# Performance work log

Measured on AMD Instinct MI355X. Metric: run time of the kernel, lower is better.

Reference implementation:

```python
import jax, jax.numpy as jnp
import numpy as np

N_NODES = 100000


def setup_inputs() -> dict:
    key = jax.random.key(0)
    k1, k2, k3, k4, k5 = jax.random.split(key, 5)
    n_feat, n_class = 128, 64
    E = 3200000
    x = jax.random.normal(k1, (N_NODES, n_feat), dtype=jnp.float32)
    edge_index = jax.random.randint(k2, (2, E), 0, N_NODES, dtype=jnp.int64)
    edge_weight = jax.random.uniform(k3, (E,), dtype=jnp.float32)
    # GCNConv params: glorot weight [in, out], zero-init bias (use small random for a non-trivial check)
    limit = float(np.sqrt(6.0 / (n_feat + n_class)))
    W = jax.random.uniform(k4, (n_feat, n_class), dtype=jnp.float32, minval=-limit, maxval=limit)
    b = jax.random.normal(k5, (n_class,), dtype=jnp.float32) * 0.01
    return {"x": x, "edge_index": edge_index, "edge_weight": edge_weight, "W": W, "b": b}


def _gcn_norm(edge_index, edge_weight, n):
    # add self-loops with weight 1 (PyG default fill_value=1.0)
    loop = jnp.arange(n, dtype=edge_index.dtype)
    row = jnp.concatenate([edge_index[0], loop])
    col = jnp.concatenate([edge_index[1], loop])
    w = jnp.concatenate([edge_weight, jnp.ones((n,), dtype=edge_weight.dtype)])
    deg = jax.ops.segment_sum(w, col, num_segments=n)  # in-degree by weight
    dis = jnp.where(deg > 0, jax.lax.rsqrt(jnp.where(deg > 0, deg, 1.0)), 0.0)
    norm = dis[row] * w * dis[col]
    return row, col, norm


def reference(x, edge_index, edge_weight, W, b):
    n = x.shape[0]
    row, col, norm = _gcn_norm(edge_index, edge_weight, n)
    h = x @ W  # linear transform before propagation, as in PyG GCNConv
    # gather source messages, scale by norm, scatter-add into targets
    msgs = h[row] * norm[:, None]          # [E+N, n_class]
    out = jax.ops.segment_sum(msgs, col, num_segments=n)
    return jax.nn.sigmoid(out + b)
```

## Files before the change

### kernel.cpp

```cpp
#include <hip/hip_runtime.h>
#include <hip/hip_bf16.h>
#include <math.h>


#define BLK 256
#define BBLK 1024
#define ABLK 1024
#define NBINBLK 512
#define NGRP 8
#define NB  512
#define CAPG 1024
#define CPB_MAX 200
#define PAD 76

typedef unsigned long long u64;
typedef unsigned int u32;
typedef unsigned short u16;
typedef unsigned char u8;
typedef _Float16 half8 __attribute__((ext_vector_type(8)));
typedef float f32x4 __attribute__((ext_vector_type(4)));

__global__ __launch_bounds__(BLK) void k_prep(const float* __restrict__ W,
                                              u16* __restrict__ WT,
                                              u32* __restrict__ cursor) {
    int gid = blockIdx.x * BLK + threadIdx.x;
    int gsz = gridDim.x * BLK;
    for (int i = gid; i < NB * NGRP; i += gsz) cursor[i] = 0u;
    for (int i = gid; i < 64 * 128; i += gsz) {
        int nn = i >> 7, k = i & 127;
        _Float16 h = (_Float16)W[k * 64 + nn];
        WT[nn * 128 + k] = *(u16*)&h;
    }
}

__global__ __launch_bounds__(BBLK) void k_bin(const int* __restrict__ row,
                                              const int* __restrict__ col,
                                              const float* __restrict__ w,
                                              u32* cursor,
                                              u64* __restrict__ staged,
                                              int E, int cpb, int nbins, int bpb) {
    __shared__ u32 hist[NB];
    __shared__ u32 sbase[NB];
    int t = threadIdx.x;
    int grp = blockIdx.x & (NGRP - 1);
    for (int j = t; j < NB; j += BBLK) hist[j] = 0;
    __syncthreads();
    int e0 = blockIdx.x * bpb;
    int e1 = min(e0 + bpb, E);
    int e = e0 + t;
    for (; e + 3 * BBLK < e1; e += 4 * BBLK) {
        int c0 = col[e];
        int c1 = col[e + BBLK];
        int c2 = col[e + 2 * BBLK];
        int c3 = col[e + 3 * BBLK];
        atomicAdd(&hist[(u32)c0 / (u32)cpb], 1u);
        atomicAdd(&hist[(u32)c1 / (u32)cpb], 1u);
        atomicAdd(&hist[(u32)c2 / (u32)cpb], 1u);
        atomicAdd(&hist[(u32)c3 / (u32)cpb], 1u);
    }
    for (; e < e1; e += BBLK)
        atomicAdd(&hist[(u32)col[e] / (u32)cpb], 1u);
    __syncthreads();
    for (int j = t; j < nbins; j += BBLK) {
        u32 h = hist[j];
        sbase[j] = h ? atomicAdd(&cursor[j * NGRP + grp], h) : 0u;
        hist[j] = 0u;
    }
    __syncthreads();
    e = e0 + t;
    for (; e + 3 * BBLK < e1; e += 4 * BBLK) {
#pragma unroll
        for (int j = 0; j < 4; j++) {
            int ee = e + j * BBLK;
            u32 c = (u32)col[ee];
            u32 bin = c / (u32)cpb;
            u32 colrel = c - bin * (u32)cpb;
            u32 wfix = (u32)(w[ee] * 65535.0f + 0.5f);
            u32 rel = sbase[bin] + atomicAdd(&hist[bin], 1u);
            if (rel < (u32)CAPG)
                staged[((size_t)bin * NGRP + grp) * CAPG + rel] =
                    (u64)((u32)row[ee] & 0xFFFFFu) | ((u64)colrel << 20)
                    | ((u64)wfix << 32);
        }
    }
    for (; e < e1; e += BBLK) {
        u32 c = (u32)col[e];
        u32 bin = c / (u32)cpb;
        u32 colrel = c - bin * (u32)cpb;
        u32 wfix = (u32)(w[e] * 65535.0f + 0.5f);
        u32 rel = sbase[bin] + atomicAdd(&hist[bin], 1u);
        if (rel < (u32)CAPG)
            staged[((size_t)bin * NGRP + grp) * CAPG + rel] =
                (u64)((u32)row[e] & 0xFFFFFu) | ((u64)colrel << 20)
                | ((u64)wfix << 32);
    }
}

__global__ __launch_bounds__(BLK) void k_deg(const u32* __restrict__ cursor,
                                             const u64* __restrict__ staged,
                                             float* __restrict__ dis,
                                             int N, int cpb) {
    __shared__ u32 deg[CPB_MAX];
    int bin = blockIdx.x, t = threadIdx.x;
    if (t < CPB_MAX) deg[t] = 0u;
    __syncthreads();
    for (int g = 0; g < NGRP; g++) {
        int ne = min((int)cursor[bin * NGRP + g], CAPG);
        size_t base = ((size_t)bin * NGRP + g) * CAPG;
        for (int i = t; i < ne; i += BLK) {
            u64 s = staged[base + i];
            atomicAdd(&deg[(u32)(s >> 20) & 0xFFFu], (u32)(s >> 32));
        }
    }
    __syncthreads();
    for (int j = t; j < cpb; j += BLK) {
        int c = bin * cpb + j;
        if (c < N)
            dis[c] = rsqrtf(1.0f + (float)deg[j] * (1.0f / 65535.0f));
    }
}

static __device__ __forceinline__ u16 f2bf(float f) {
    __hip_bfloat16 h = __float2bfloat16(f);
    return *(u16*)&h;
}

__global__ __launch_bounds__(BLK) void k_gemmM(const float* __restrict__ x,
                                               const u16* __restrict__ WT,
                                               const float* __restrict__ dis,
                                               u16* __restrict__ hs, int n) {
    __shared__ __attribute__((aligned(16))) _Float16 sx[64 * 136];
    __shared__ __attribute__((aligned(16))) _Float16 sw[64 * 136];
    __shared__ float sdis[64];
    int t = threadIdx.x;
    int m0 = blockIdx.x * 64;
    for (int i = t; i < 2048; i += BLK) {
        int r = i >> 5, q = i & 31;
        int gr = m0 + r;
        float4 v = make_float4(0.f, 0.f, 0.f, 0.f);
        if (gr < n) v = ((const float4*)x)[(size_t)gr * 32 + q];
        _Float16* dst = &sx[r * 136 + q * 4];
        dst[0] = (_Float16)v.x; dst[1] = (_Float16)v.y;
        dst[2] = (_Float16)v.z; dst[3] = (_Float16)v.w;
    }
    for (int i = t; i < 2048; i += BLK) {
        int nn = i >> 5, q = i & 31;
        ushort4 v = ((const ushort4*)WT)[nn * 32 + q];
        u16* dst = (u16*)&sw[nn * 136 + q * 4];
        dst[0] = v.x; dst[1] = v.y; dst[2] = v.z; dst[3] = v.w;
    }
    if (t < 64) sdis[t] = (m0 + t < n) ? dis[m0 + t] : 0.f;
    __syncthreads();
    int wv = t >> 6, lane = t & 63;
    int quad = lane >> 4, l16 = lane & 15;
    int mrow = wv * 16 + l16;
    half8 af[4];
#pragma unroll
    for (int kt = 0; kt < 4; kt++)
        af[kt] = *(const half8*)&sx[mrow * 136 + kt * 32 + quad * 8];
#pragma unroll
    for (int n0t = 0; n0t < 4; n0t++) {
        f32x4 acc = {0.f, 0.f, 0.f, 0.f};
#pragma unroll
        for (int kt = 0; kt < 4; kt++) {
            half8 bf_ = *(const half8*)&sw[(n0t * 16 + l16) * 136 + kt * 32 + quad * 8];
            acc = __builtin_amdgcn_mfma_f32_16x16x32_f16(af[kt], bf_, acc, 0, 0, 0);
        }
#pragma unroll
        for (int r = 0; r < 4; r++) {
            int mr = wv * 16 + quad * 4 + r;
            int gr = m0 + mr;
            if (gr < n)
                hs[(size_t)gr * 64 + n0t * 16 + l16] = f2bf(acc[r] * sdis[mr]);
        }
    }
}

__global__ __launch_bounds__(ABLK) void k_buildagg(const u32* __restrict__ cursor,
                                                   const u64* __restrict__ staged,
                                                   const uint2* __restrict__ hs64,
                                                   const float* __restrict__ dis,
                                                   const float* __restrict__ b,
                                                   float* __restrict__ out,
                                                   int N, int cpb) {
    __shared__ u32 cnt[CPB_MAX];
    __shared__ u32 lbkt[CPB_MAX * PAD];
    int bin = blockIdx.x, t = threadIdx.x;
    if (t < CPB_MAX) cnt[t] = 0u;
    __syncthreads();
    for (int g = 0; g < NGRP; g++) {
        int ne = min((int)cursor[bin * NGRP + g], CAPG);
        size_t base = ((size_t)bin * NGRP + g) * CAPG;
        for (int i = t; i < ne; i += ABLK) {
            u64 s = staged[base + i];
            u32 colrel = (u32)(s >> 20) & 0xFFFu;
            u32 wfix = (u32)(s >> 32);
            u32 rk = atomicAdd(&cnt[colrel], 1u);
            if (rk < (u32)PAD)
                lbkt[colrel * PAD + rk] = ((u32)s & 0xFFFFFu) | ((wfix >> 1) << 17);
        }
    }
    __syncthreads();
    int wv = t >> 6;
    int lane = t & 63;
    int q = lane >> 4, fp = lane & 15;
    const float WS = 1.0f / 32767.0f;
    for (int colrel = wv; colrel < cpb; colrel += (ABLK / 64)) {
        int node = bin * cpb + colrel;
        if (node >= N) break;
        int cc = (int)cnt[colrel];
        if (cc > PAD) cc = PAD;
        const u32* bkt = &lbkt[colrel * PAD];
        float a0, a1, a2, a3;
        if (q == 0) {
            uint2 s = hs64[((size_t)node << 4) + fp];
            a0 = __uint_as_float(s.x << 16);
            a1 = __uint_as_float(s.x & 0xFFFF0000u);
            a2 = __uint_as_float(s.y << 16);
            a3 = __uint_as_float(s.y & 0xFFFF0000u);
        } else {
            a0 = a1 = a2 = a3 = 0.f;
        }
        for (int e = 0; e < cc; e += 4) {
            int idx = e + q;
            u32 p = (idx < cc) ? bkt[idx] : 0u;
            float w = (float)(p >> 17) * WS;
            uint2 g = hs64[((size_t)(p & 0x1FFFFu) << 4) + fp];
            a0 = fmaf(__uint_as_float(g.x << 16), w, a0);
            a1 = fmaf(__uint_as_float(g.x & 0xFFFF0000u), w, a1);
            a2 = fmaf(__uint_as_float(g.y << 16), w, a2);
            a3 = fmaf(__uint_as_float(g.y & 0xFFFF0000u), w, a3);
        }
        a0 += __shfl_down(a0, 16); a1 += __shfl_down(a1, 16);
        a2 += __shfl_down(a2, 16); a3 += __shfl_down(a3, 16);
        a0 += __shfl_down(a0, 32); a1 += __shfl_down(a1, 32);
        a2 += __shfl_down(a2, 32); a3 += __shfl_down(a3, 32);
        if (q == 0) {
            float d = dis[node];
            float4 bv = ((const float4*)b)[fp];
            float4 o;
            o.x = 1.0f / (1.0f + __expf(-(d * a0 + bv.x)));
            o.y = 1.0f / (1.0f + __expf(-(d * a1 + bv.y)));
            o.z = 1.0f / (1.0f + __expf(-(d * a2 + bv.z)));
            o.w = 1.0f / (1.0f + __expf(-(d * a3 + bv.w)));
            ((float4*)out)[((size_t)node << 4) + fp] = o;
        }
    }
}

static inline size_t align_up(size_t v, size_t a) { return (v + a - 1) & ~(a - 1); }

extern "C" void kernel_launch(void* const* d_in, const int* in_sizes, int n_in,
                              void* d_out, int out_size, void* d_ws, size_t ws_size,
                              hipStream_t stream) {
    const float* x  = (const float*)d_in[0];
    const int*   ei = (const int*)d_in[1];
    const float* ew = (const float*)d_in[2];
    const float* W  = (const float*)d_in[3];
    const float* b  = (const float*)d_in[4];
    float* out = (float*)d_out;

    const int E = in_sizes[2];
    const int N = in_sizes[0] / 128;

    const int* row = ei;
    const int* col = ei + E;

    const int cpb   = (N + NB - 1) / NB;
    const int nbins = (N + cpb - 1) / cpb;
    const int bpb   = (E + NBINBLK - 1) / NBINBLK;

    char* p = (char*)d_ws;
    u32* cursor = (u32*)p; p += align_up((size_t)NB * NGRP * 4, 256);
    u64* staged = (u64*)p; p += align_up((size_t)NB * NGRP * CAPG * 8, 256);
    float* dis  = (float*)p; p += align_up((size_t)N * 4, 256);
    u16* hs     = (u16*)p; p += align_up((size_t)N * 64 * 2, 256);
    u16* WT     = (u16*)p; p += align_up((size_t)64 * 128 * 2, 256);
    (void)ws_size;

    k_prep<<<8, BLK, 0, stream>>>(W, WT, cursor);
    k_bin<<<NBINBLK, BBLK, 0, stream>>>(row, col, ew, cursor, staged,
                                        E, cpb, nbins, bpb);
    k_deg<<<nbins, BLK, 0, stream>>>(cursor, staged, dis, N, cpb);
    k_gemmM<<<(N + 63) / 64, BLK, 0, stream>>>(x, WT, dis, hs, N);
    k_buildagg<<<nbins, ABLK, 0, stream>>>(cursor, staged, (const uint2*)hs,
                                           dis, b, out, N, cpb);
}
```

Baseline: 268.2 us.

## Fuse all stages into one cooperative persistent kernel with grid syncs

Replaces the five separate launches (prep, bin, degree, GEMM, aggregate) with one cooperative kernel that uses grid-wide syncs between phases and loops over virtual blocks. The source-side normalisation is moved from the GEMM epilogue into the per-edge weights during bucket building, so the GEMM no longer depends on dis. The GEMM is also reorganised so each of 16 waves computes one 16x16 output tile of a 64-row block. This removes launch gaps and inter-kernel drain, but limits the grid to resident blocks of 1024 threads with about 62KB of LDS each, and adds grid-sync overhead plus a per-edge dis gather.

```diff
diff --git a/kernel.cpp b/kernel.cpp
--- a/kernel.cpp
+++ b/kernel.cpp
@@ -1,249 +1,255 @@
 #include <hip/hip_runtime.h>
+#include <hip/hip_cooperative_groups.h>
 #include <hip/hip_bf16.h>
 #include <math.h>
 
 
-#define BLK 256
-#define BBLK 1024
-#define ABLK 1024
+#define NB  512
 #define NBINBLK 512
 #define NGRP 8
-#define NB  512
 #define CAPG 1024
 #define CPB_MAX 200
 #define PAD 76
+#define MTHR 1024
 
 typedef unsigned long long u64;
 typedef unsigned int u32;
 typedef unsigned short u16;
-typedef unsigned char u8;
 typedef _Float16 half8 __attribute__((ext_vector_type(8)));
 typedef float f32x4 __attribute__((ext_vector_type(4)));
 
-__global__ __launch_bounds__(BLK) void k_prep(const float* __restrict__ W,
-                                              u16* __restrict__ WT,
-                                              u32* __restrict__ cursor) {
-    int gid = blockIdx.x * BLK + threadIdx.x;
-    int gsz = gridDim.x * BLK;
+namespace cg = cooperative_groups;
+
+static __device__ __forceinline__ u16 f2bf(float f) {
+    __hip_bfloat16 h = __float2bfloat16(f);
+    return *(u16*)&h;
+}
+static __device__ __forceinline__ float bfl(u32 v) { return __uint_as_float(v << 16); }
+static __device__ __forceinline__ float bfh(u32 v) { return __uint_as_float(v & 0xFFFF0000u); }
+
+__global__ __launch_bounds__(MTHR, 8) void k_mega(
+    const float* __restrict__ x, const int* __restrict__ ei,
+    const float* __restrict__ ew, const float* __restrict__ W,
+    const float* __restrict__ b, float* __restrict__ out,
+    u32* cursor, u64* __restrict__ staged, float* __restrict__ dis,
+    u16* __restrict__ hs, u16* __restrict__ WT,
+    int E, int N, int cpb, int nbins, int bpb, int ntiles)
+{
+    __shared__ __attribute__((aligned(16))) char smem[61952];
+    cg::grid_group grid = cg::this_grid();
+    const int t = threadIdx.x;
+    const int blk = blockIdx.x;
+    const int gsz = gridDim.x * MTHR;
+    const int gid = blk * MTHR + t;
+    const int* rowp = ei;
+    const int* colp = ei + E;
+
     for (int i = gid; i < NB * NGRP; i += gsz) cursor[i] = 0u;
     for (int i = gid; i < 64 * 128; i += gsz) {
         int nn = i >> 7, k = i & 127;
         _Float16 h = (_Float16)W[k * 64 + nn];
         WT[nn * 128 + k] = *(u16*)&h;
     }
-}
-
-__global__ __launch_bounds__(BBLK) void k_bin(const int* __restrict__ row,
-                                              const int* __restrict__ col,
-                                              const float* __restrict__ w,
-                                              u32* cursor,
-                                              u64* __restrict__ staged,
-                                              int E, int cpb, int nbins, int bpb) {
-    __shared__ u32 hist[NB];
-    __shared__ u32 sbase[NB];
-    int t = threadIdx.x;
-    int grp = blockIdx.x & (NGRP - 1);
-    for (int j = t; j < NB; j += BBLK) hist[j] = 0;
-    __syncthreads();
-    int e0 = blockIdx.x * bpb;
-    int e1 = min(e0 + bpb, E);
-    int e = e0 + t;
-    for (; e + 3 * BBLK < e1; e += 4 * BBLK) {
-        int c0 = col[e];
-        int c1 = col[e + BBLK];
-        int c2 = col[e + 2 * BBLK];
-        int c3 = col[e + 3 * BBLK];
-        atomicAdd(&hist[(u32)c0 / (u32)cpb], 1u);
-        atomicAdd(&hist[(u32)c1 / (u32)cpb], 1u);
-        atomicAdd(&hist[(u32)c2 / (u32)cpb], 1u);
-        atomicAdd(&hist[(u32)c3 / (u32)cpb], 1u);
-    }
-    for (; e < e1; e += BBLK)
-        atomicAdd(&hist[(u32)col[e] / (u32)cpb], 1u);
-    __syncthreads();
-    for (int j = t; j < nbins; j += BBLK) {
-        u32 h = hist[j];
-        sbase[j] = h ? atomicAdd(&cursor[j * NGRP + grp], h) : 0u;
-        hist[j] = 0u;
-    }
-    __syncthreads();
-    e = e0 + t;
-    for (; e + 3 * BBLK < e1; e += 4 * BBLK) {
-#pragma unroll
-        for (int j = 0; j < 4; j++) {
-            int ee = e + j * BBLK;
-            u32 c = (u32)col[ee];
+    __threadfence();
+    grid.sync();
+
+    for (int vb = blk; vb < NBINBLK; vb += gridDim.x) {
+        u32* hist = (u32*)smem;
+        u32* sbase = hist + NB;
+        int grp = vb & (NGRP - 1);
+        __syncthreads();
+        for (int j = t; j < NB; j += MTHR) hist[j] = 0u;
+        __syncthreads();
+        int e0 = vb * bpb;
+        int e1 = min(e0 + bpb, E);
+        int e = e0 + t;
+        for (; e + 3 * MTHR < e1; e += 4 * MTHR) {
+            int c0 = colp[e];
+            int c1 = colp[e + MTHR];
+            int c2 = colp[e + 2 * MTHR];
+            int c3 = colp[e + 3 * MTHR];
+            atomicAdd(&hist[(u32)c0 / (u32)cpb], 1u);
+            atomicAdd(&hist[(u32)c1 / (u32)cpb], 1u);
+            atomicAdd(&hist[(u32)c2 / (u32)cpb], 1u);
+            atomicAdd(&hist[(u32)c3 / (u32)cpb], 1u);
+        }
+        for (; e < e1; e += MTHR)
+            atomicAdd(&hist[(u32)colp[e] / (u32)cpb], 1u);
+        __syncthreads();
+        for (int j = t; j < nbins; j += MTHR) {
+            u32 h = hist[j];
+            sbase[j] = h ? atomicAdd(&cursor[j * NGRP + grp], h) : 0u;
+            hist[j] = 0u;
+        }
+        __syncthreads();
+        e = e0 + t;
+        for (; e + 3 * MTHR < e1; e += 4 * MTHR) {
+#pragma unroll
+            for (int j = 0; j < 4; j++) {
+                int ee = e + j * MTHR;
+                u32 c = (u32)colp[ee];
+                u32 bin = c / (u32)cpb;
+                u32 colrel = c - bin * (u32)cpb;
+                u32 wfix = (u32)(ew[ee] * 65535.0f + 0.5f);
+                u32 rel = sbase[bin] + atomicAdd(&hist[bin], 1u);
+                if (rel < (u32)CAPG)
+                    staged[((size_t)bin * NGRP + grp) * CAPG + rel] =
+                        (u64)((u32)rowp[ee] & 0xFFFFFu) | ((u64)colrel << 20)
+                        | ((u64)wfix << 32);
+            }
+        }
+        for (; e < e1; e += MTHR) {
+            u32 c = (u32)colp[e];
             u32 bin = c / (u32)cpb;
             u32 colrel = c - bin * (u32)cpb;
-            u32 wfix = (u32)(w[ee] * 65535.0f + 0.5f);
+            u32 wfix = (u32)(ew[e] * 65535.0f + 0.5f);
             u32 rel = sbase[bin] + atomicAdd(&hist[bin], 1u);
             if (rel < (u32)CAPG)
                 staged[((size_t)bin * NGRP + grp) * CAPG + rel] =
-                    (u64)((u32)row[ee] & 0xFFFFFu) | ((u64)colrel << 20)
+                    (u64)((u32)rowp[e] & 0xFFFFFu) | ((u64)colrel << 20)
                     | ((u64)wfix << 32);
         }
     }
-    for (; e < e1; e += BBLK) {
-        u32 c = (u32)col[e];
-        u32 bin = c / (u32)cpb;
-        u32 colrel = c - bin * (u32)cpb;
-        u32 wfix = (u32)(w[e] * 65535.0f + 0.5f);
-        u32 rel = sbase[bin] + atomicAdd(&hist[bin], 1u);
-        if (rel < (u32)CAPG)
-            staged[((size_t)bin * NGRP + grp) * CAPG + rel] =
-                (u64)((u32)row[e] & 0xFFFFFu) | ((u64)colrel << 20)
-                | ((u64)wfix << 32);
-    }
-}
-
-__global__ __launch_bounds__(BLK) void k_deg(const u32* __restrict__ cursor,
-                                             const u64* __restrict__ staged,
-                                             float* __restrict__ dis,
-                                             int N, int cpb) {
-    __shared__ u32 deg[CPB_MAX];
-    int bin = blockIdx.x, t = threadIdx.x;
-    if (t < CPB_MAX) deg[t] = 0u;
+    __threadfence();
+    grid.sync();
+
+    for (int vbin = blk; vbin < nbins; vbin += gridDim.x) {
+        u32* sdeg = (u32*)smem;
+        __syncthreads();
+        for (int j = t; j < CPB_MAX; j += MTHR) sdeg[j] = 0u;
+        __syncthreads();
+        for (int g = 0; g < NGRP; g++) {
+            int ne = min((int)cursor[vbin * NGRP + g], CAPG);
+            size_t base = ((size_t)vbin * NGRP + g) * CAPG;
+            for (int i = t; i < ne; i += MTHR) {
+                u64 s = staged[base + i];
+                atomicAdd(&sdeg[(u32)(s >> 20) & 0xFFFu], (u32)(s >> 32));
+            }
+        }
+        __syncthreads();
+        for (int j = t; j < cpb; j += MTHR) {
+            int c = vbin * cpb + j;
+            if (c < N)
+                dis[c] = rsqrtf(1.0f + (float)sdeg[j] * (1.0f / 65535.0f));
+        }
+    }
     __syncthreads();
-    for (int g = 0; g < NGRP; g++) {
-        int ne = min((int)cursor[bin * NGRP + g], CAPG);
-        size_t base = ((size_t)bin * NGRP + g) * CAPG;
-        for (int i = t; i < ne; i += BLK) {
-            u64 s = staged[base + i];
-            atomicAdd(&deg[(u32)(s >> 20) & 0xFFFu], (u32)(s >> 32));
-        }
-    }
-    __syncthreads();
-    for (int j = t; j < cpb; j += BLK) {
-        int c = bin * cpb + j;
-        if (c < N)
-            dis[c] = rsqrtf(1.0f + (float)deg[j] * (1.0f / 65535.0f));
-    }
-}
-
-static __device__ __forceinline__ u16 f2bf(float f) {
-    __hip_bfloat16 h = __float2bfloat16(f);
-    return *(u16*)&h;
-}
-
-__global__ __launch_bounds__(BLK) void k_gemmM(const float* __restrict__ x,
-                                               const u16* __restrict__ WT,
-                                               const float* __restrict__ dis,
-                                               u16* __restrict__ hs, int n) {
-    __shared__ __attribute__((aligned(16))) _Float16 sx[64 * 136];
-    __shared__ __attribute__((aligned(16))) _Float16 sw[64 * 136];
-    __shared__ float sdis[64];
-    int t = threadIdx.x;
-    int m0 = blockIdx.x * 64;
-    for (int i = t; i < 2048; i += BLK) {
-        int r = i >> 5, q = i & 31;
-        int gr = m0 + r;
-        float4 v = make_float4(0.f, 0.f, 0.f, 0.f);
-        if (gr < n) v = ((const float4*)x)[(size_t)gr * 32 + q];
-        _Float16* dst = &sx[r * 136 + q * 4];
-        dst[0] = (_Float16)v.x; dst[1] = (_Float16)v.y;
-        dst[2] = (_Float16)v.z; dst[3] = (_Float16)v.w;
-    }
-    for (int i = t; i < 2048; i += BLK) {
-        int nn = i >> 5, q = i & 31;
-        ushort4 v = ((const ushort4*)WT)[nn * 32 + q];
-        u16* dst = (u16*)&sw[nn * 136 + q * 4];
-        dst[0] = v.x; dst[1] = v.y; dst[2] = v.z; dst[3] = v.w;
-    }
-    if (t < 64) sdis[t] = (m0 + t < n) ? dis[m0 + t] : 0.f;
-    __syncthreads();
-    int wv = t >> 6, lane = t & 63;
-    int quad = lane >> 4, l16 = lane & 15;
-    int mrow = wv * 16 + l16;
-    half8 af[4];
-#pragma unroll
-    for (int kt = 0; kt < 4; kt++)
-        af[kt] = *(const half8*)&sx[mrow * 136 + kt * 32 + quad * 8];
-#pragma unroll
-    for (int n0t = 0; n0t < 4; n0t++) {
-        f32x4 acc = {0.f, 0.f, 0.f, 0.f};
-#pragma unroll
-        for (int kt = 0; kt < 4; kt++) {
-            half8 bf_ = *(const half8*)&sw[(n0t * 16 + l16) * 136 + kt * 32 + quad * 8];
-            acc = __builtin_amdgcn_mfma_f32_16x16x32_f16(af[kt], bf_, acc, 0, 0, 0);
-        }
-#pragma unroll
-        for (int r = 0; r < 4; r++) {
-            int mr = wv * 16 + quad * 4 + r;
-            int gr = m0 + mr;
-            if (gr < n)
-                hs[(size_t)gr * 64 + n0t * 16 + l16] = f2bf(acc[r] * sdis[mr]);
-        }
-    }
-}
-
-__global__ __launch_bounds__(ABLK) void k_buildagg(const u32* __restrict__ cursor,
-                                                   const u64* __restrict__ staged,
-                                                   const uint2* __restrict__ hs64,
-                                                   const float* __restrict__ dis,
-                                                   const float* __restrict__ b,
-                                                   float* __restrict__ out,
-                                                   int N, int cpb) {
-    __shared__ u32 cnt[CPB_MAX];
-    __shared__ u32 lbkt[CPB_MAX * PAD];
-    int bin = blockIdx.x, t = threadIdx.x;
-    if (t < CPB_MAX) cnt[t] = 0u;
-    __syncthreads();
-    for (int g = 0; g < NGRP; g++) {
-        int ne = min((int)cursor[bin * NGRP + g], CAPG);
-        size_t base = ((size_t)bin * NGRP + g) * CAPG;
-        for (int i = t; i < ne; i += ABLK) {
-            u64 s = staged[base + i];
-            u32 colrel = (u32)(s >> 20) & 0xFFFu;
-            u32 wfix = (u32)(s >> 32);
-            u32 rk = atomicAdd(&cnt[colrel], 1u);
-            if (rk < (u32)PAD)
-                lbkt[colrel * PAD + rk] = ((u32)s & 0xFFFFFu) | ((wfix >> 1) << 17);
-        }
-    }
-    __syncthreads();
-    int wv = t >> 6;
-    int lane = t & 63;
-    int q = lane >> 4, fp = lane & 15;
-    const float WS = 1.0f / 32767.0f;
-    for (int colrel = wv; colrel < cpb; colrel += (ABLK / 64)) {
-        int node = bin * cpb + colrel;
-        if (node >= N) break;
-        int cc = (int)cnt[colrel];
-        if (cc > PAD) cc = PAD;
-        const u32* bkt = &lbkt[colrel * PAD];
-        float a0, a1, a2, a3;
-        if (q == 0) {
-            uint2 s = hs64[((size_t)node << 4) + fp];
-            a0 = __uint_as_float(s.x << 16);
-            a1 = __uint_as_float(s.x & 0xFFFF0000u);
-            a2 = __uint_as_float(s.y << 16);
-            a3 = __uint_as_float(s.y & 0xFFFF0000u);
-        } else {
-            a0 = a1 = a2 = a3 = 0.f;
-        }
-        for (int e = 0; e < cc; e += 4) {
-            int idx = e + q;
-            u32 p = (idx < cc) ? bkt[idx] : 0u;
-            float w = (float)(p >> 17) * WS;
-            uint2 g = hs64[((size_t)(p & 0x1FFFFu) << 4) + fp];
-            a0 = fmaf(__uint_as_float(g.x << 16), w, a0);
-            a1 = fmaf(__uint_as_float(g.x & 0xFFFF0000u), w, a1);
-            a2 = fmaf(__uint_as_float(g.y << 16), w, a2);
-            a3 = fmaf(__uint_as_float(g.y & 0xFFFF0000u), w, a3);
-        }
-        a0 += __shfl_down(a0, 16); a1 += __shfl_down(a1, 16);
-        a2 += __shfl_down(a2, 16); a3 += __shfl_down(a3, 16);
-        a0 += __shfl_down(a0, 32); a1 += __shfl_down(a1, 32);
-        a2 += __shfl_down(a2, 32); a3 += __shfl_down(a3, 32);
-        if (q == 0) {
-            float d = dis[node];
-            float4 bv = ((const float4*)b)[fp];
-            float4 o;
-            o.x = 1.0f / (1.0f + __expf(-(d * a0 + bv.x)));
-            o.y = 1.0f / (1.0f + __expf(-(d * a1 + bv.y)));
-            o.z = 1.0f / (1.0f + __expf(-(d * a2 + bv.z)));
-            o.w = 1.0f / (1.0f + __expf(-(d * a3 + bv.w)));
-            ((float4*)out)[((size_t)node << 4) + fp] = o;
+
+    {
+        _Float16* sx = (_Float16*)smem;
+        _Float16* sw = (_Float16*)(smem + 17408);
+        for (int i = t; i < 2048; i += MTHR) {
+            int nn = i >> 5, q = i & 31;
+            ushort4 v = ((const ushort4*)WT)[nn * 32 + q];
+            u16* dst = (u16*)&sw[nn * 136 + q * 4];
+            dst[0] = v.x; dst[1] = v.y; dst[2] = v.z; dst[3] = v.w;
+        }
+        int wv = t >> 6, lane = t & 63;
+        int quad = lane >> 4, l16 = lane & 15;
+        int rg = wv >> 2, n0t = wv & 3;
+        int mrow = rg * 16 + l16;
+        for (int tile = blk; tile < ntiles; tile += gridDim.x) {
+            __syncthreads();
+            int m0 = tile * 64;
+            for (int i = t; i < 2048; i += MTHR) {
+                int r = i >> 5, q = i & 31;
+                int gr = m0 + r;
+                float4 v = make_float4(0.f, 0.f, 0.f, 0.f);
+                if (gr < N) v = ((const float4*)x)[(size_t)gr * 32 + q];
+                _Float16* dst = &sx[r * 136 + q * 4];
+                dst[0] = (_Float16)v.x; dst[1] = (_Float16)v.y;
+                dst[2] = (_Float16)v.z; dst[3] = (_Float16)v.w;
+            }
+            __syncthreads();
+            half8 af[4];
+#pragma unroll
+            for (int kt = 0; kt < 4; kt++)
+                af[kt] = *(const half8*)&sx[mrow * 136 + kt * 32 + quad * 8];
+            f32x4 acc = {0.f, 0.f, 0.f, 0.f};
+#pragma unroll
+            for (int kt = 0; kt < 4; kt++) {
+                half8 bf_ = *(const half8*)&sw[(n0t * 16 + l16) * 136 + kt * 32 + quad * 8];
+                acc = __builtin_amdgcn_mfma_f32_16x16x32_f16(af[kt], bf_, acc, 0, 0, 0);
+            }
+#pragma unroll
+            for (int r = 0; r < 4; r++) {
+                int mr = rg * 16 + quad * 4 + r;
+                int gr = m0 + mr;
+                if (gr < N)
+                    hs[(size_t)gr * 64 + n0t * 16 + l16] = f2bf(acc[r]);
+            }
+        }
+    }
+    __threadfence();
+    grid.sync();
+
+    {
+        const uint2* hs64 = (const uint2*)hs;
+        u32* cnt = (u32*)smem;
+        u32* lbkt = cnt + 256;
+        const float WS = 1.0f / 32767.0f;
+        int wv = t >> 6, lane = t & 63;
+        int q = lane >> 4, fp = lane & 15;
+        for (int vbin = blk; vbin < nbins; vbin += gridDim.x) {
+            __syncthreads();
+            if (t < CPB_MAX) cnt[t] = 0u;
+            __syncthreads();
+            for (int g = 0; g < NGRP; g++) {
+                int ne = min((int)cursor[vbin * NGRP + g], CAPG);
+                size_t base = ((size_t)vbin * NGRP + g) * CAPG;
+                for (int i = t; i < ne; i += MTHR) {
+                    u64 s = staged[base + i];
+                    u32 colrel = (u32)(s >> 20) & 0xFFFu;
+                    u32 rowid = (u32)s & 0xFFFFFu;
+                    float wp = (float)(u32)(s >> 32) * (1.0f / 65535.0f) * dis[rowid];
+                    u32 q15 = (u32)(wp * 32767.0f + 0.5f);
+                    u32 rk = atomicAdd(&cnt[colrel], 1u);
+                    if (rk < (u32)PAD)
+                        lbkt[colrel * PAD + rk] = rowid | (q15 << 17);
+                }
+            }
+            __syncthreads();
+            for (int colrel = wv; colrel < cpb; colrel += (MTHR / 64)) {
+                int node = vbin * cpb + colrel;
+                if (node >= N) break;
+                int cc = (int)cnt[colrel];
+                if (cc > PAD) cc = PAD;
+                const u32* bkt = &lbkt[colrel * PAD];
+                float dnode = dis[node];
+                float a0, a1, a2, a3;
+                if (q == 0) {
+                    uint2 s = hs64[((size_t)node << 4) + fp];
+                    a0 = bfl(s.x) * dnode;
+                    a1 = bfh(s.x) * dnode;
+                    a2 = bfl(s.y) * dnode;
+                    a3 = bfh(s.y) * dnode;
+                } else {
+                    a0 = a1 = a2 = a3 = 0.f;
+                }
+                for (int e = 0; e < cc; e += 4) {
+                    int idx = e + q;
+                    u32 p = (idx < cc) ? bkt[idx] : 0u;
+                    float w = (float)(p >> 17) * WS;
+                    uint2 g = hs64[((size_t)(p & 0x1FFFFu) << 4) + fp];
+                    a0 = fmaf(bfl(g.x), w, a0);
+                    a1 = fmaf(bfh(g.x), w, a1);
+                    a2 = fmaf(bfl(g.y), w, a2);
+                    a3 = fmaf(bfh(g.y), w, a3);
+                }
+                a0 += __shfl_down(a0, 16); a1 += __shfl_down(a1, 16);
+                a2 += __shfl_down(a2, 16); a3 += __shfl_down(a3, 16);
+                a0 += __shfl_down(a0, 32); a1 += __shfl_down(a1, 32);
+                a2 += __shfl_down(a2, 32); a3 += __shfl_down(a3, 32);
+                if (q == 0) {
+                    float4 bv = ((const float4*)b)[fp];
+                    float4 o;
+                    o.x = 1.0f / (1.0f + __expf(-(dnode * a0 + bv.x)));
+                    o.y = 1.0f / (1.0f + __expf(-(dnode * a1 + bv.y)));
+                    o.z = 1.0f / (1.0f + __expf(-(dnode * a2 + bv.z)));
+                    o.w = 1.0f / (1.0f + __expf(-(dnode * a3 + bv.w)));
+                    ((float4*)out)[((size_t)node << 4) + fp] = o;
+                }
+            }
         }
     }
 }
@@ -260,15 +266,13 @@
     const float* b  = (const float*)d_in[4];
     float* out = (float*)d_out;
 
-    const int E = in_sizes[2];
-    const int N = in_sizes[0] / 128;
-
-    const int* row = ei;
-    const int* col = ei + E;
-
-    const int cpb   = (N + NB - 1) / NB;
-    const int nbins = (N + cpb - 1) / cpb;
-    const int bpb   = (E + NBINBLK - 1) / NBINBLK;
+    int E = in_sizes[2];
+    int N = in_sizes[0] / 128;
+
+    int cpb   = (N + NB - 1) / NB;
+    int nbins = (N + cpb - 1) / cpb;
+    int bpb   = (E + NBINBLK - 1) / NBINBLK;
+    int ntiles = (N + 63) / 64;
 
     char* p = (char*)d_ws;
     u32* cursor = (u32*)p; p += align_up((size_t)NB * NGRP * 4, 256);
@@ -278,11 +282,17 @@
     u16* WT     = (u16*)p; p += align_up((size_t)64 * 128 * 2, 256);
     (void)ws_size;
 
-    k_prep<<<8, BLK, 0, stream>>>(W, WT, cursor);
-    k_bin<<<NBINBLK, BBLK, 0, stream>>>(row, col, ew, cursor, staged,
-                                        E, cpb, nbins, bpb);
-    k_deg<<<nbins, BLK, 0, stream>>>(cursor, staged, dis, N, cpb);
-    k_gemmM<<<(N + 63) / 64, BLK, 0, stream>>>(x, WT, dis, hs, N);
-    k_buildagg<<<nbins, ABLK, 0, stream>>>(cursor, staged, (const uint2*)hs,
-                                           dis, b, out, N, cpb);
+    int blocksPerCU = 0;
+    hipOccupancyMaxActiveBlocksPerMultiprocessor(&blocksPerCU, k_mega, MTHR, 0);
+    if (blocksPerCU < 1) blocksPerCU = 1;
+    int grid = blocksPerCU * 256;
+    if (grid > NBINBLK) grid = NBINBLK;
+
+    void* kargs[] = {
+        (void*)&x, (void*)&ei, (void*)&ew, (void*)&W, (void*)&b, (void*)&out,
+        (void*)&cursor, (void*)&staged, (void*)&dis, (void*)&hs, (void*)&WT,
+        (void*)&E, (void*)&N, (void*)&cpb, (void*)&nbins, (void*)&bpb,
+        (void*)&ntiles
+    };
+    hipLaunchCooperativeKernel(k_mega, dim3(grid), dim3(MTHR), kargs, 0, stream);
 }
```

After: 710.9 us. 2.65x slower.

## Fuse edge binning with GEMM in one launch and move degree normalization

Applied to the files above, without the earlier changes.

Edge binning and the feature GEMM now run in a single kernel, with blocks interleaved so both stages can overlap on the GPU. The GEMM no longer needs the degree scaling, so it no longer depends on the binning stage. Degrees are accumulated with global atomics during binning, which replaces the separate staged-buffer degree pass with a small elementwise kernel. The source-side norm is folded into the per-edge quantized weight in the aggregation kernel. The cost is heavier global atomic traffic on deg and a 15-bit quantization of the combined weight.

```diff
diff --git a/kernel.cpp b/kernel.cpp
--- a/kernel.cpp
+++ b/kernel.cpp
@@ -4,8 +4,7 @@
 
 
 #define BLK 256
-#define BBLK 1024
-#define ABLK 1024
+#define MBLK 1024
 #define NBINBLK 512
 #define NGRP 8
 #define NB  512
@@ -16,16 +15,24 @@
 typedef unsigned long long u64;
 typedef unsigned int u32;
 typedef unsigned short u16;
-typedef unsigned char u8;
 typedef _Float16 half8 __attribute__((ext_vector_type(8)));
 typedef float f32x4 __attribute__((ext_vector_type(4)));
 
+static __device__ __forceinline__ u16 f2bf(float f) {
+    __hip_bfloat16 h = __float2bfloat16(f);
+    return *(u16*)&h;
+}
+static __device__ __forceinline__ float bfl(u32 v) { return __uint_as_float(v << 16); }
+static __device__ __forceinline__ float bfh(u32 v) { return __uint_as_float(v & 0xFFFF0000u); }
+
 __global__ __launch_bounds__(BLK) void k_prep(const float* __restrict__ W,
                                               u16* __restrict__ WT,
-                                              u32* __restrict__ cursor) {
+                                              u32* __restrict__ cursor,
+                                              u32* __restrict__ deg, int N) {
     int gid = blockIdx.x * BLK + threadIdx.x;
     int gsz = gridDim.x * BLK;
     for (int i = gid; i < NB * NGRP; i += gsz) cursor[i] = 0u;
+    for (int i = gid; i < N; i += gsz) deg[i] = 0u;
     for (int i = gid; i < 64 * 128; i += gsz) {
         int nn = i >> 7, k = i & 127;
         _Float16 h = (_Float16)W[k * 64 + nn];
@@ -33,133 +40,115 @@
     }
 }
 
-__global__ __launch_bounds__(BBLK) void k_bin(const int* __restrict__ row,
-                                              const int* __restrict__ col,
-                                              const float* __restrict__ w,
-                                              u32* cursor,
-                                              u64* __restrict__ staged,
-                                              int E, int cpb, int nbins, int bpb) {
-    __shared__ u32 hist[NB];
-    __shared__ u32 sbase[NB];
+__global__ __launch_bounds__(MBLK, 2) void k_binGemm(
+    const int* __restrict__ row, const int* __restrict__ col,
+    const float* __restrict__ w, u32* cursor, u64* __restrict__ staged,
+    u32* __restrict__ deg, const float* __restrict__ x,
+    const u16* __restrict__ WT, u16* __restrict__ hs,
+    int E, int N, int cpb, int nbins, int bpb, int ntiles) {
+    __shared__ __attribute__((aligned(16))) char smem[34816];
+    int b = blockIdx.x;
     int t = threadIdx.x;
-    int grp = blockIdx.x & (NGRP - 1);
-    for (int j = t; j < NB; j += BBLK) hist[j] = 0;
-    __syncthreads();
-    int e0 = blockIdx.x * bpb;
-    int e1 = min(e0 + bpb, E);
-    int e = e0 + t;
-    for (; e + 3 * BBLK < e1; e += 4 * BBLK) {
-        int c0 = col[e];
-        int c1 = col[e + BBLK];
-        int c2 = col[e + 2 * BBLK];
-        int c3 = col[e + 3 * BBLK];
-        atomicAdd(&hist[(u32)c0 / (u32)cpb], 1u);
-        atomicAdd(&hist[(u32)c1 / (u32)cpb], 1u);
-        atomicAdd(&hist[(u32)c2 / (u32)cpb], 1u);
-        atomicAdd(&hist[(u32)c3 / (u32)cpb], 1u);
-    }
-    for (; e < e1; e += BBLK)
-        atomicAdd(&hist[(u32)col[e] / (u32)cpb], 1u);
-    __syncthreads();
-    for (int j = t; j < nbins; j += BBLK) {
-        u32 h = hist[j];
-        sbase[j] = h ? atomicAdd(&cursor[j * NGRP + grp], h) : 0u;
-        hist[j] = 0u;
-    }
-    __syncthreads();
-    e = e0 + t;
-    for (; e + 3 * BBLK < e1; e += 4 * BBLK) {
-#pragma unroll
-        for (int j = 0; j < 4; j++) {
-            int ee = e + j * BBLK;
-            u32 c = (u32)col[ee];
+
+    bool isBin;
+    int vbin = 0, vtile = 0;
+    if (512 + ntiles >= 2048) {
+        if (b < 2048 && (b & 3) == 0) { isBin = true; vbin = b >> 2; }
+        else {
+            isBin = false;
+            vtile = (b < 2048) ? (b - ((b >> 2) + 1)) : (b - 512);
+        }
+    } else {
+        if (b < NBINBLK) { isBin = true; vbin = b; }
+        else { isBin = false; vtile = b - NBINBLK; }
+    }
+
+    if (isBin) {
+        u32* hist = (u32*)smem;
+        u32* sbase = hist + NB;
+        int grp = vbin & (NGRP - 1);
+        for (int j = t; j < NB; j += MBLK) hist[j] = 0u;
+        __syncthreads();
+        int e0 = vbin * bpb;
+        int e1 = min(e0 + bpb, E);
+        int e = e0 + t;
+        for (; e + 3 * MBLK < e1; e += 4 * MBLK) {
+            int c0 = col[e];
+            int c1 = col[e + MBLK];
+            int c2 = col[e + 2 * MBLK];
+            int c3 = col[e + 3 * MBLK];
+            atomicAdd(&hist[(u32)c0 / (u32)cpb], 1u);
+            atomicAdd(&hist[(u32)c1 / (u32)cpb], 1u);
+            atomicAdd(&hist[(u32)c2 / (u32)cpb], 1u);
+            atomicAdd(&hist[(u32)c3 / (u32)cpb], 1u);
+        }
+        for (; e < e1; e += MBLK)
+            atomicAdd(&hist[(u32)col[e] / (u32)cpb], 1u);
+        __syncthreads();
+        for (int j = t; j < nbins; j += MBLK) {
+            u32 h = hist[j];
+            sbase[j] = h ? atomicAdd(&cursor[j * NGRP + grp], h) : 0u;
+            hist[j] = 0u;
+        }
+        __syncthreads();
+        e = e0 + t;
+        for (; e + 3 * MBLK < e1; e += 4 * MBLK) {
+#pragma unroll
+            for (int j = 0; j < 4; j++) {
+                int ee = e + j * MBLK;
+                u32 c = (u32)col[ee];
+                u32 bin = c / (u32)cpb;
+                u32 colrel = c - bin * (u32)cpb;
+                u32 wfix = (u32)(w[ee] * 65535.0f + 0.5f);
+                atomicAdd(&deg[c], wfix);
+                u32 rel = sbase[bin] + atomicAdd(&hist[bin], 1u);
+                if (rel < (u32)CAPG)
+                    staged[((size_t)bin * NGRP + grp) * CAPG + rel] =
+                        (u64)((u32)row[ee] & 0xFFFFFu) | ((u64)colrel << 20)
+                        | ((u64)wfix << 32);
+            }
+        }
+        for (; e < e1; e += MBLK) {
+            u32 c = (u32)col[e];
             u32 bin = c / (u32)cpb;
             u32 colrel = c - bin * (u32)cpb;
-            u32 wfix = (u32)(w[ee] * 65535.0f + 0.5f);
+            u32 wfix = (u32)(w[e] * 65535.0f + 0.5f);
+            atomicAdd(&deg[c], wfix);
             u32 rel = sbase[bin] + atomicAdd(&hist[bin], 1u);
             if (rel < (u32)CAPG)
                 staged[((size_t)bin * NGRP + grp) * CAPG + rel] =
-                    (u64)((u32)row[ee] & 0xFFFFFu) | ((u64)colrel << 20)
+                    (u64)((u32)row[e] & 0xFFFFFu) | ((u64)colrel << 20)
                     | ((u64)wfix << 32);
         }
-    }
-    for (; e < e1; e += BBLK) {
-        u32 c = (u32)col[e];
-        u32 bin = c / (u32)cpb;
-        u32 colrel = c - bin * (u32)cpb;
-        u32 wfix = (u32)(w[e] * 65535.0f + 0.5f);
-        u32 rel = sbase[bin] + atomicAdd(&hist[bin], 1u);
-        if (rel < (u32)CAPG)
-            staged[((size_t)bin * NGRP + grp) * CAPG + rel] =
-                (u64)((u32)row[e] & 0xFFFFFu) | ((u64)colrel << 20)
-                | ((u64)wfix << 32);
-    }
-}
-
-__global__ __launch_bounds__(BLK) void k_deg(const u32* __restrict__ cursor,
-                                             const u64* __restrict__ staged,
-                                             float* __restrict__ dis,
-                                             int N, int cpb) {
-    __shared__ u32 deg[CPB_MAX];
-    int bin = blockIdx.x, t = threadIdx.x;
-    if (t < CPB_MAX) deg[t] = 0u;
-    __syncthreads();
-    for (int g = 0; g < NGRP; g++) {
-        int ne = min((int)cursor[bin * NGRP + g], CAPG);
-        size_t base = ((size_t)bin * NGRP + g) * CAPG;
-        for (int i = t; i < ne; i += BLK) {
-            u64 s = staged[base + i];
-            atomicAdd(&deg[(u32)(s >> 20) & 0xFFFu], (u32)(s >> 32));
-        }
-    }
-    __syncthreads();
-    for (int j = t; j < cpb; j += BLK) {
-        int c = bin * cpb + j;
-        if (c < N)
-            dis[c] = rsqrtf(1.0f + (float)deg[j] * (1.0f / 65535.0f));
-    }
-}
-
-static __device__ __forceinline__ u16 f2bf(float f) {
-    __hip_bfloat16 h = __float2bfloat16(f);
-    return *(u16*)&h;
-}
-
-__global__ __launch_bounds__(BLK) void k_gemmM(const float* __restrict__ x,
-                                               const u16* __restrict__ WT,
-                                               const float* __restrict__ dis,
-                                               u16* __restrict__ hs, int n) {
-    __shared__ __attribute__((aligned(16))) _Float16 sx[64 * 136];
-    __shared__ __attribute__((aligned(16))) _Float16 sw[64 * 136];
-    __shared__ float sdis[64];
-    int t = threadIdx.x;
-    int m0 = blockIdx.x * 64;
-    for (int i = t; i < 2048; i += BLK) {
-        int r = i >> 5, q = i & 31;
-        int gr = m0 + r;
-        float4 v = make_float4(0.f, 0.f, 0.f, 0.f);
-        if (gr < n) v = ((const float4*)x)[(size_t)gr * 32 + q];
-        _Float16* dst = &sx[r * 136 + q * 4];
-        dst[0] = (_Float16)v.x; dst[1] = (_Float16)v.y;
-        dst[2] = (_Float16)v.z; dst[3] = (_Float16)v.w;
-    }
-    for (int i = t; i < 2048; i += BLK) {
-        int nn = i >> 5, q = i & 31;
-        ushort4 v = ((const ushort4*)WT)[nn * 32 + q];
-        u16* dst = (u16*)&sw[nn * 136 + q * 4];
-        dst[0] = v.x; dst[1] = v.y; dst[2] = v.z; dst[3] = v.w;
-    }
-    if (t < 64) sdis[t] = (m0 + t < n) ? dis[m0 + t] : 0.f;
-    __syncthreads();
-    int wv = t >> 6, lane = t & 63;
-    int quad = lane >> 4, l16 = lane & 15;
-    int mrow = wv * 16 + l16;
-    half8 af[4];
-#pragma unroll
-    for (int kt = 0; kt < 4; kt++)
-        af[kt] = *(const half8*)&sx[mrow * 136 + kt * 32 + quad * 8];
-#pragma unroll
-    for (int n0t = 0; n0t < 4; n0t++) {
+    } else {
+        if (vtile >= ntiles) return;
+        _Float16* sx = (_Float16*)smem;
+        _Float16* sw = (_Float16*)(smem + 17408);
+        int m0 = vtile * 64;
+        for (int i = t; i < 2048; i += MBLK) {
+            int r = i >> 5, q = i & 31;
+            int gr = m0 + r;
+            float4 v = make_float4(0.f, 0.f, 0.f, 0.f);
+            if (gr < N) v = ((const float4*)x)[(size_t)gr * 32 + q];
+            _Float16* dst = &sx[r * 136 + q * 4];
+            dst[0] = (_Float16)v.x; dst[1] = (_Float16)v.y;
+            dst[2] = (_Float16)v.z; dst[3] = (_Float16)v.w;
+        }
+        for (int i = t; i < 2048; i += MBLK) {
+            int nn = i >> 5, q = i & 31;
+            ushort4 v = ((const ushort4*)WT)[nn * 32 + q];
+            u16* dst = (u16*)&sw[nn * 136 + q * 4];
+            dst[0] = v.x; dst[1] = v.y; dst[2] = v.z; dst[3] = v.w;
+        }
+        __syncthreads();
+        int wv = t >> 6, lane = t & 63;
+        int quad = lane >> 4, l16 = lane & 15;
+        int rg = wv >> 2, n0t = wv & 3;
+        int mrow = rg * 16 + l16;
+        half8 af[4];
+#pragma unroll
+        for (int kt = 0; kt < 4; kt++)
+            af[kt] = *(const half8*)&sx[mrow * 136 + kt * 32 + quad * 8];
         f32x4 acc = {0.f, 0.f, 0.f, 0.f};
 #pragma unroll
         for (int kt = 0; kt < 4; kt++) {
@@ -168,21 +157,28 @@
         }
 #pragma unroll
         for (int r = 0; r < 4; r++) {
-            int mr = wv * 16 + quad * 4 + r;
+            int mr = rg * 16 + quad * 4 + r;
             int gr = m0 + mr;
-            if (gr < n)
-                hs[(size_t)gr * 64 + n0t * 16 + l16] = f2bf(acc[r] * sdis[mr]);
-        }
-    }
-}
-
-__global__ __launch_bounds__(ABLK) void k_buildagg(const u32* __restrict__ cursor,
-                                                   const u64* __restrict__ staged,
-                                                   const uint2* __restrict__ hs64,
-                                                   const float* __restrict__ dis,
-                                                   const float* __restrict__ b,
-                                                   float* __restrict__ out,
-                                                   int N, int cpb) {
+            if (gr < N)
+                hs[(size_t)gr * 64 + n0t * 16 + l16] = f2bf(acc[r]);
+        }
+    }
+}
+
+__global__ __launch_bounds__(BLK) void k_dis(const u32* __restrict__ deg,
+                                             float* __restrict__ dis, int N) {
+    int i = blockIdx.x * BLK + threadIdx.x;
+    if (i < N)
+        dis[i] = rsqrtf(1.0f + (float)deg[i] * (1.0f / 65535.0f));
+}
+
+__global__ __launch_bounds__(MBLK, 8) void k_agg(const u32* __restrict__ cursor,
+                                                 const u64* __restrict__ staged,
+                                                 const uint2* __restrict__ hs64,
+                                                 const float* __restrict__ dis,
+                                                 const float* __restrict__ b,
+                                                 float* __restrict__ out,
+                                                 int N, int cpb) {
     __shared__ u32 cnt[CPB_MAX];
     __shared__ u32 lbkt[CPB_MAX * PAD];
     int bin = blockIdx.x, t = threadIdx.x;
@@ -191,13 +187,15 @@
     for (int g = 0; g < NGRP; g++) {
         int ne = min((int)cursor[bin * NGRP + g], CAPG);
         size_t base = ((size_t)bin * NGRP + g) * CAPG;
-        for (int i = t; i < ne; i += ABLK) {
+        for (int i = t; i < ne; i += MBLK) {
             u64 s = staged[base + i];
             u32 colrel = (u32)(s >> 20) & 0xFFFu;
-            u32 wfix = (u32)(s >> 32);
+            u32 rowid = (u32)s & 0xFFFFFu;
+            float wp = (float)(u32)(s >> 32) * (1.0f / 65535.0f) * dis[rowid];
+            u32 q15 = (u32)(wp * 32767.0f + 0.5f);
             u32 rk = atomicAdd(&cnt[colrel], 1u);
             if (rk < (u32)PAD)
-                lbkt[colrel * PAD + rk] = ((u32)s & 0xFFFFFu) | ((wfix >> 1) << 17);
+                lbkt[colrel * PAD + rk] = rowid | (q15 << 17);
         }
     }
     __syncthreads();
@@ -205,19 +203,20 @@
     int lane = t & 63;
     int q = lane >> 4, fp = lane & 15;
     const float WS = 1.0f / 32767.0f;
-    for (int colrel = wv; colrel < cpb; colrel += (ABLK / 64)) {
+    for (int colrel = wv; colrel < cpb; colrel += (MBLK / 64)) {
         int node = bin * cpb + colrel;
         if (node >= N) break;
         int cc = (int)cnt[colrel];
         if (cc > PAD) cc = PAD;
         const u32* bkt = &lbkt[colrel * PAD];
+        float dnode = dis[node];
         float a0, a1, a2, a3;
         if (q == 0) {
             uint2 s = hs64[((size_t)node << 4) + fp];
-            a0 = __uint_as_float(s.x << 16);
-            a1 = __uint_as_float(s.x & 0xFFFF0000u);
-            a2 = __uint_as_float(s.y << 16);
-            a3 = __uint_as_float(s.y & 0xFFFF0000u);
+            a0 = bfl(s.x) * dnode;
+            a1 = bfh(s.x) * dnode;
+            a2 = bfl(s.y) * dnode;
+            a3 = bfh(s.y) * dnode;
         } else {
             a0 = a1 = a2 = a3 = 0.f;
         }
@@ -226,23 +225,22 @@
             u32 p = (idx < cc) ? bkt[idx] : 0u;
             float w = (float)(p >> 17) * WS;
             uint2 g = hs64[((size_t)(p & 0x1FFFFu) << 4) + fp];
-            a0 = fmaf(__uint_as_float(g.x << 16), w, a0);
-            a1 = fmaf(__uint_as_float(g.x & 0xFFFF0000u), w, a1);
-            a2 = fmaf(__uint_as_float(g.y << 16), w, a2);
-            a3 = fmaf(__uint_as_float(g.y & 0xFFFF0000u), w, a3);
+            a0 = fmaf(bfl(g.x), w, a0);
+            a1 = fmaf(bfh(g.x), w, a1);
+            a2 = fmaf(bfl(g.y), w, a2);
+            a3 = fmaf(bfh(g.y), w, a3);
         }
         a0 += __shfl_down(a0, 16); a1 += __shfl_down(a1, 16);
         a2 += __shfl_down(a2, 16); a3 += __shfl_down(a3, 16);
         a0 += __shfl_down(a0, 32); a1 += __shfl_down(a1, 32);
         a2 += __shfl_down(a2, 32); a3 += __shfl_down(a3, 32);
         if (q == 0) {
-            float d = dis[node];
             float4 bv = ((const float4*)b)[fp];
             float4 o;
-            o.x = 1.0f / (1.0f + __expf(-(d * a0 + bv.x)));
-            o.y = 1.0f / (1.0f + __expf(-(d * a1 + bv.y)));
-            o.z = 1.0f / (1.0f + __expf(-(d * a2 + bv.z)));
-            o.w = 1.0f / (1.0f + __expf(-(d * a3 + bv.w)));
+            o.x = 1.0f / (1.0f + __expf(-(dnode * a0 + bv.x)));
+            o.y = 1.0f / (1.0f + __expf(-(dnode * a1 + bv.y)));
+            o.z = 1.0f / (1.0f + __expf(-(dnode * a2 + bv.z)));
+            o.w = 1.0f / (1.0f + __expf(-(dnode * a3 + bv.w)));
             ((float4*)out)[((size_t)node << 4) + fp] = o;
         }
     }
@@ -269,6 +267,7 @@
     const int cpb   = (N + NB - 1) / NB;
     const int nbins = (N + cpb - 1) / cpb;
     const int bpb   = (E + NBINBLK - 1) / NBINBLK;
+    const int ntiles = (N + 63) / 64;
 
     char* p = (char*)d_ws;
     u32* cursor = (u32*)p; p += align_up((size_t)NB * NGRP * 4, 256);
@@ -276,13 +275,15 @@
     float* dis  = (float*)p; p += align_up((size_t)N * 4, 256);
     u16* hs     = (u16*)p; p += align_up((size_t)N * 64 * 2, 256);
     u16* WT     = (u16*)p; p += align_up((size_t)64 * 128 * 2, 256);
+    u32* deg    = (u32*)p; p += align_up((size_t)N * 4, 256);
     (void)ws_size;
 
-    k_prep<<<8, BLK, 0, stream>>>(W, WT, cursor);
-    k_bin<<<NBINBLK, BBLK, 0, stream>>>(row, col, ew, cursor, staged,
-                                        E, cpb, nbins, bpb);
-    k_deg<<<nbins, BLK, 0, stream>>>(cursor, staged, dis, N, cpb);
-    k_gemmM<<<(N + 63) / 64, BLK, 0, stream>>>(x, WT, dis, hs, N);
-    k_buildagg<<<nbins, ABLK, 0, stream>>>(cursor, staged, (const uint2*)hs,
-                                           dis, b, out, N, cpb);
-}
+    k_prep<<<64, BLK, 0, stream>>>(W, WT, cursor, deg, N);
+    k_binGemm<<<NBINBLK + ntiles, MBLK, 0, stream>>>(row, col, ew, cursor,
+                                                     staged, deg, x, WT, hs,
+                                                     E, N, cpb, nbins, bpb,
+                                                     ntiles);
+    k_dis<<<(N + BLK - 1) / BLK, BLK, 0, stream>>>(deg, dis, N);
+    k_agg<<<nbins, MBLK, 0, stream>>>(cursor, staged, (const uint2*)hs,
+                                      dis, b, out, N, cpb);
+}
```

Measured after the change: 452.5 us. 68.8% more time.
